# Kernel tuning notes

Measured on AMD Instinct MI355X. Metric: run time of the kernel, lower is better.

## Reference

```python
import jax, jax.numpy as jnp
import numpy as np
import math

B, L, C, H = 8, 1024, 1024, 8
EPS = 1e-5

def setup_inputs() -> dict:
    key = jax.random.key(0)
    ks = jax.random.split(key, 5)
    s = 0.02
    return {
        "x": jax.random.normal(ks[0], (B, L, C), dtype=jnp.float32),
        "ln_g": jnp.ones((C,), dtype=jnp.float32),
        "ln_b": jnp.zeros((C,), dtype=jnp.float32),
        "w_qkv": jax.random.normal(ks[1], (C, 3 * C), dtype=jnp.float32) * s,
        "b_qkv": jax.random.normal(ks[2], (3 * C,), dtype=jnp.float32) * s,
        "w_out": jax.random.normal(ks[3], (C, C), dtype=jnp.float32) * s,
        "b_out": jax.random.normal(ks[4], (C,), dtype=jnp.float32) * s,
    }

def reference(x, ln_g, ln_b, w_qkv, b_qkv, w_out, b_out):
    bs, length, width = x.shape
    ch = width // H
    # LayerNorm over channels
    mu = jnp.mean(x, axis=-1, keepdims=True)
    var = jnp.mean(jnp.square(x - mu), axis=-1, keepdims=True)
    xn = (x - mu) * jax.lax.rsqrt(var + EPS) * ln_g + ln_b
    # fused QKV projection
    qkv = jnp.einsum('blc,cd->bld', xn, w_qkv) + b_qkv  # [B, L, 3C]
    q, k, v = jnp.split(qkv, 3, axis=2)                 # each [B, L, C]
    scale = 1.0 / math.sqrt(math.sqrt(ch))
    # faithful raw row-major reshape as in the torch .view call
    q = (q * scale).reshape(bs * H, length, ch)
    k = (k * scale).reshape(bs * H, length, ch)
    v = v.reshape(bs * H, length, ch)
    w = jnp.einsum('bqc,bkc->bqk', q, k)                # [B*H, L, L] score matrix
    w = jax.nn.softmax(w.astype(jnp.float32), axis=-1).astype(q.dtype)
    attn = jnp.einsum('bqk,bkc->bqc', w, v).reshape(bs, length, -1)
    out = jnp.einsum('blc,cd->bld', attn, w_out) + b_out + xn  # residual uses normalized x
    return out
```

## Files before the change

### kernel.cpp

```cpp
#include <hip/hip_runtime.h>
#include <hip/hip_bf16.h>


typedef __attribute__((ext_vector_type(8))) short short8;
typedef __attribute__((ext_vector_type(4))) float f32x4;

#define QK_SCALE 0.29730177875068026f

__device__ __forceinline__ float bf2f(ushort u) {
    union { float f; unsigned int i; } c; c.i = ((unsigned int)u) << 16; return c.f;
}
__device__ __forceinline__ ushort f2bf(float f) {
    union { float f; unsigned int i; } c; c.f = f;
    unsigned int x = c.i;
    return (ushort)((x + 0x7FFFu + ((x >> 16) & 1u)) >> 16);
}

__device__ __forceinline__ void gload_lds16(const ushort* g, ushort* l) {
    __builtin_amdgcn_global_load_lds(
        (const __attribute__((address_space(1))) unsigned int*)g,
        (__attribute__((address_space(3))) unsigned int*)l, 16, 0, 0);
}

__global__ __launch_bounds__(256) void prep_kernel(
    const float* __restrict__ x, const float* __restrict__ g,
    const float* __restrict__ b, ushort* __restrict__ xn,
    const float* __restrict__ w_qkv, ushort* __restrict__ wqkvT,
    const float* __restrict__ w_out, ushort* __restrict__ woutT) {
    __shared__ ushort t[32][33];
    int bid = blockIdx.x;
    int tid = threadIdx.x;
    if (bid < 2048) {
        int w = tid >> 6, lane = tid & 63;
        int row = bid * 4 + w;
        const float* xr = x + (size_t)row * 1024;
        float v[4][4];
        float s1 = 0.f, s2 = 0.f;
#pragma unroll
        for (int j = 0; j < 4; j++) {
            float4 t4 = *(const float4*)(xr + lane * 4 + j * 256);
            v[j][0] = t4.x; v[j][1] = t4.y; v[j][2] = t4.z; v[j][3] = t4.w;
#pragma unroll
            for (int e = 0; e < 4; e++) { s1 += v[j][e]; s2 += v[j][e] * v[j][e]; }
        }
#pragma unroll
        for (int m = 32; m >= 1; m >>= 1) { s1 += __shfl_xor(s1, m); s2 += __shfl_xor(s2, m); }
        float mu = s1 * (1.0f / 1024.0f);
        float var = s2 * (1.0f / 1024.0f) - mu * mu;
        float rs = rsqrtf(var + 1e-5f);
#pragma unroll
        for (int j = 0; j < 4; j++) {
            int c0 = lane * 4 + j * 256;
            float4 gg = *(const float4*)(g + c0);
            float4 bb = *(const float4*)(b + c0);
            float gA[4] = {gg.x, gg.y, gg.z, gg.w};
            float bA[4] = {bb.x, bb.y, bb.z, bb.w};
            ushort o[4];
#pragma unroll
            for (int e = 0; e < 4; e++) o[e] = f2bf((v[j][e] - mu) * rs * gA[e] + bA[e]);
            uint2 pk;
            pk.x = (uint)o[0] | ((uint)o[1] << 16);
            pk.y = (uint)o[2] | ((uint)o[3] << 16);
            *(uint2*)(xn + (size_t)row * 1024 + c0) = pk;
        }
    } else {
        const float* in; ushort* out; int R, Cc, bx, by;
        if (bid < 5120) {
            int tt = bid - 2048;
            in = w_qkv; out = wqkvT; R = 1024; Cc = 3072;
            bx = (tt % 96) * 32; by = (tt / 96) * 32;
        } else {
            int tt = bid - 5120;
            in = w_out; out = woutT; R = 1024; Cc = 1024;
            bx = (tt % 32) * 32; by = (tt / 32) * 32;
        }
        int tx = tid & 31, ty = tid >> 5;
#pragma unroll
        for (int j = 0; j < 32; j += 8)
            t[ty + j][tx] = f2bf(in[(size_t)(by + ty + j) * Cc + bx + tx]);
        __syncthreads();
#pragma unroll
        for (int j = 0; j < 32; j += 8)
            out[(size_t)(bx + ty + j) * R + by + tx] = t[tx][ty + j];
    }
}

__global__ __launch_bounds__(256) void transpose_head(
    const ushort* __restrict__ in, ushort* __restrict__ out) {
    __shared__ ushort t[32][33];
    int h = blockIdx.z;
    int j0 = blockIdx.y * 32;
    int d0 = blockIdx.x * 32;
    int tx = threadIdx.x & 31, ty = threadIdx.x >> 5;
    const ushort* src = in + (size_t)h * 131072;
    ushort* dst = out + (size_t)h * 131072;
#pragma unroll
    for (int j = 0; j < 32; j += 8)
        t[ty + j][tx] = src[(size_t)(j0 + ty + j) * 128 + d0 + tx];
    __syncthreads();
#pragma unroll
    for (int j = 0; j < 32; j += 8)
        dst[(size_t)(d0 + ty + j) * 1024 + j0 + tx] = t[tx][ty + j];
}

__device__ __forceinline__ void stage8(const ushort* __restrict__ Ab,
                                       const ushort* __restrict__ Bb, int t2,
                                       ushort* AsD, ushort* BsD, int tid) {
    const ushort* As_src = Ab + t2 * 64;
    const ushort* Bs_src = Bb + t2 * 64;
#pragma unroll
    for (int i = 0; i < 4; i++) {
        int lin = i * 256 + tid;
        int r = lin >> 3, p = lin & 7;
        int l = p ^ (r & 7);
        gload_lds16(As_src + (size_t)r * 1024 + l * 8, &AsD[lin * 8]);
    }
#pragma unroll
    for (int i = 0; i < 4; i++) {
        int lin = i * 256 + tid;
        int r = lin >> 3, p = lin & 7;
        int l = p ^ (r & 7);
        gload_lds16(Bs_src + (size_t)r * 1024 + l * 8, &BsD[lin * 8]);
    }
}

__global__ __launch_bounds__(256, 2) void gemm_qkv(
    const ushort* __restrict__ A, const ushort* __restrict__ Bt,
    const float* __restrict__ bias, ushort* __restrict__ out0,
    ushort* __restrict__ out1, ushort* __restrict__ out2) {
    __shared__ __align__(16) ushort As[2][128 * 64];
    __shared__ __align__(16) ushort Bs[2][128 * 64];

    int tid = threadIdx.x;
    int lane = tid & 63, w = tid >> 6;
    int l15 = lane & 15, q4 = lane >> 4;
    int wrM = (w >> 1) * 64;
    int wcN = (w & 1) * 64;

    int bid = blockIdx.x;
    int xcd = bid & 7;
    int i = bid >> 3;
    int by = xcd * 8 + (i & 7);
    int bx = i >> 3;
    int rowBase = by * 128, colBase = bx * 128;

    const ushort* Ab = A + (size_t)rowBase * 1024;
    const ushort* Bb = Bt + (size_t)colBase * 1024;

    f32x4 acc[4][4];
    f32x4 zero = {0.f, 0.f, 0.f, 0.f};
#pragma unroll
    for (int mi = 0; mi < 4; mi++)
#pragma unroll
        for (int ni = 0; ni < 4; ni++) acc[mi][ni] = zero;

    stage8(Ab, Bb, 0, &As[0][0], &Bs[0][0], tid);
    stage8(Ab, Bb, 1, &As[1][0], &Bs[1][0], tid);
    asm volatile("s_waitcnt vmcnt(8)" ::: "memory");
    __builtin_amdgcn_s_barrier();

    for (int t = 0; t < 16; ++t) {
        const int cur = t & 1;
        const ushort* Ac = &As[cur][0];
        const ushort* Bc = &Bs[cur][0];

        short8 aF[4][2], bF[4][2];
#pragma unroll
        for (int kk = 0; kk < 2; kk++) {
#pragma unroll
            for (int mi = 0; mi < 4; mi++) {
                int r = wrM + mi * 16 + l15;
                aF[mi][kk] = *(const short8*)&Ac[r * 64 + ((kk * 4 + q4) ^ (r & 7)) * 8];
            }
#pragma unroll
            for (int ni = 0; ni < 4; ni++) {
                int r = wcN + ni * 16 + l15;
                bF[ni][kk] = *(const short8*)&Bc[r * 64 + ((kk * 4 + q4) ^ (r & 7)) * 8];
            }
        }

        __builtin_amdgcn_s_setprio(1);
#pragma unroll
        for (int mi = 0; mi < 4; mi++)
#pragma unroll
            for (int ni = 0; ni < 4; ni++)
                acc[mi][ni] = __builtin_amdgcn_mfma_f32_16x16x32_bf16(
                    aF[mi][0], bF[ni][0], acc[mi][ni], 0, 0, 0);
        __builtin_amdgcn_s_setprio(0);

        asm volatile("s_waitcnt lgkmcnt(0)" ::: "memory");
        __builtin_amdgcn_s_barrier();
        if (t < 14) stage8(Ab, Bb, t + 2, &As[cur][0], &Bs[cur][0], tid);

        __builtin_amdgcn_s_setprio(1);
#pragma unroll
        for (int mi = 0; mi < 4; mi++)
#pragma unroll
            for (int ni = 0; ni < 4; ni++)
                acc[mi][ni] = __builtin_amdgcn_mfma_f32_16x16x32_bf16(
                    aF[mi][1], bF[ni][1], acc[mi][ni], 0, 0, 0);
        __builtin_amdgcn_s_setprio(0);

        if (t < 15) {
            if (t < 14) asm volatile("s_waitcnt vmcnt(8)" ::: "memory");
            else        asm volatile("s_waitcnt vmcnt(0)" ::: "memory");
            __builtin_amdgcn_s_barrier();
        }
    }

#pragma unroll
    for (int ni = 0; ni < 4; ni++) {
        int col = colBase + wcN + ni * 16 + l15;
        float bv = bias[col];
        float sc = (col < 2048) ? QK_SCALE : 1.0f;
        int bsel = col >> 10, cc = col & 1023;
        ushort* dst = (bsel == 0) ? out0 : ((bsel == 1) ? out1 : out2);
#pragma unroll
        for (int mi = 0; mi < 4; mi++) {
            f32x4 a = acc[mi][ni];
#pragma unroll
            for (int r = 0; r < 4; r++) {
                int row = rowBase + wrM + mi * 16 + q4 * 4 + r;
                dst[(size_t)row * 1024 + cc] = f2bf((a[r] + bv) * sc);
            }
        }
    }
}

__global__ __launch_bounds__(256, 2) void gemm_out(
    const ushort* __restrict__ A, const ushort* __restrict__ Bt,
    const float* __restrict__ bias, const ushort* __restrict__ resid,
    float* __restrict__ outf) {
    __shared__ __align__(16) ushort As[2][128 * 64];
    __shared__ __align__(16) ushort Bs[2][128 * 64];

    int tid = threadIdx.x;
    int lane = tid & 63, w = tid >> 6;
    int l15 = lane & 15, q4 = lane >> 4;
    int wrM = (w >> 1) * 64;
    int wcN = (w & 1) * 64;

    int bid = blockIdx.x;
    int xcd = bid & 7;
    int i = bid >> 3;
    int by = xcd * 8 + (i & 7);
    int bx = i >> 3;
    int rowBase = by * 128, colBase = bx * 128;

    const ushort* Ab = A + (size_t)rowBase * 1024;
    const ushort* Bb = Bt + (size_t)colBase * 1024;

    f32x4 acc[4][4];
    f32x4 zero = {0.f, 0.f, 0.f, 0.f};
#pragma unroll
    for (int mi = 0; mi < 4; mi++)
#pragma unroll
        for (int ni = 0; ni < 4; ni++) acc[mi][ni] = zero;

    stage8(Ab, Bb, 0, &As[0][0], &Bs[0][0], tid);
    stage8(Ab, Bb, 1, &As[1][0], &Bs[1][0], tid);
    asm volatile("s_waitcnt vmcnt(8)" ::: "memory");
    __builtin_amdgcn_s_barrier();

    for (int t = 0; t < 16; ++t) {
        const int cur = t & 1;
        const ushort* Ac = &As[cur][0];
        const ushort* Bc = &Bs[cur][0];

        short8 aF[4][2], bF[4][2];
#pragma unroll
        for (int kk = 0; kk < 2; kk++) {
#pragma unroll
            for (int mi = 0; mi < 4; mi++) {
                int r = wrM + mi * 16 + l15;
                aF[mi][kk] = *(const short8*)&Ac[r * 64 + ((kk * 4 + q4) ^ (r & 7)) * 8];
            }
#pragma unroll
            for (int ni = 0; ni < 4; ni++) {
                int r = wcN + ni * 16 + l15;
                bF[ni][kk] = *(const short8*)&Bc[r * 64 + ((kk * 4 + q4) ^ (r & 7)) * 8];
            }
        }

        __builtin_amdgcn_s_setprio(1);
#pragma unroll
        for (int mi = 0; mi < 4; mi++)
#pragma unroll
            for (int ni = 0; ni < 4; ni++)
                acc[mi][ni] = __builtin_amdgcn_mfma_f32_16x16x32_bf16(
                    aF[mi][0], bF[ni][0], acc[mi][ni], 0, 0, 0);
        __builtin_amdgcn_s_setprio(0);

        asm volatile("s_waitcnt lgkmcnt(0)" ::: "memory");
        __builtin_amdgcn_s_barrier();
        if (t < 14) stage8(Ab, Bb, t + 2, &As[cur][0], &Bs[cur][0], tid);

        __builtin_amdgcn_s_setprio(1);
#pragma unroll
        for (int mi = 0; mi < 4; mi++)
#pragma unroll
            for (int ni = 0; ni < 4; ni++)
                acc[mi][ni] = __builtin_amdgcn_mfma_f32_16x16x32_bf16(
                    aF[mi][1], bF[ni][1], acc[mi][ni], 0, 0, 0);
        __builtin_amdgcn_s_setprio(0);

        if (t < 15) {
            if (t < 14) asm volatile("s_waitcnt vmcnt(8)" ::: "memory");
            else        asm volatile("s_waitcnt vmcnt(0)" ::: "memory");
            __builtin_amdgcn_s_barrier();
        }
    }

#pragma unroll
    for (int ni = 0; ni < 4; ni++) {
        int col = colBase + wcN + ni * 16 + l15;
        float bv = bias[col];
#pragma unroll
        for (int mi = 0; mi < 4; mi++) {
            f32x4 a = acc[mi][ni];
#pragma unroll
            for (int r = 0; r < 4; r++) {
                int row = rowBase + wrM + mi * 16 + q4 * 4 + r;
                outf[(size_t)row * 1024 + col] =
                    a[r] + bv + bf2f(resid[(size_t)row * 1024 + col]);
            }
        }
    }
}

__device__ __forceinline__ void attn_stage(const ushort* __restrict__ Kh,
                                           const ushort* __restrict__ Vh,
                                           int kt, ushort* KsD, ushort* VtD,
                                           int tid) {
#pragma unroll
    for (int i = 0; i < 2; i++) {
        int linear = i * 512 + tid;
        int r = linear >> 4, p = linear & 15;
        int l = p ^ (r & 15);
        gload_lds16(&Kh[(size_t)(kt * 64 + r) * 128 + l * 8], &KsD[linear * 8]);
    }
#pragma unroll
    for (int i = 0; i < 2; i++) {
        int linear = i * 512 + tid;
        int d = linear >> 3, p = linear & 7;
        int c = p ^ (d & 7);
        gload_lds16(&Vh[(size_t)d * 1024 + kt * 64 + c * 8], &VtD[linear * 8]);
    }
}

__global__ __launch_bounds__(512) void attn_kernel(
    const ushort* __restrict__ qb, const ushort* __restrict__ kb,
    const ushort* __restrict__ vt, ushort* __restrict__ ob) {
    int bid = blockIdx.x;
    int xcd = bid & 7, ii = bid >> 3;
    int g = xcd * 8 + (ii >> 3);
    int qblk = ii & 7;
    const ushort* Qh = qb + (size_t)g * 131072;
    const ushort* Kh = kb + (size_t)g * 131072;
    const ushort* Vh = vt + (size_t)g * 131072;

    __shared__ __align__(16) ushort Ks[2][64 * 128];
    __shared__ __align__(16) ushort Vt[2][128 * 64];
    __shared__ __align__(16) ushort Ps[128 * 64];

    int tid = threadIdx.x, lane = tid & 63, w = tid >> 6;
    int l15 = lane & 15, q4 = lane >> 4;
    int q0 = qblk * 128;

    short8 qf[4];
#pragma unroll
    for (int ks = 0; ks < 4; ks++)
        qf[ks] = *(const short8*)&Qh[(size_t)(q0 + w * 16 + l15) * 128 + ks * 32 + q4 * 8];

    f32x4 zero = {0.f, 0.f, 0.f, 0.f};
    f32x4 o[8];
#pragma unroll
    for (int ni = 0; ni < 8; ni++) o[ni] = zero;
    float plsum[4] = {0.f, 0.f, 0.f, 0.f};

    attn_stage(Kh, Vh, 0, &Ks[0][0], &Vt[0][0], tid);
    attn_stage(Kh, Vh, 1, &Ks[1][0], &Vt[1][0], tid);
    asm volatile("s_waitcnt vmcnt(4)" ::: "memory");
    __builtin_amdgcn_s_barrier();

    for (int kt = 0; kt < 16; kt++) {
        const int cur = kt & 1;
        const ushort* Kc = &Ks[cur][0];
        const ushort* Vc = &Vt[cur][0];

        f32x4 sacc[4];
#pragma unroll
        for (int ni = 0; ni < 4; ni++) sacc[ni] = zero;
        __builtin_amdgcn_s_setprio(1);
#pragma unroll
        for (int ks = 0; ks < 4; ks++) {
#pragma unroll
            for (int ni = 0; ni < 4; ni++) {
                int r = ni * 16 + l15;
                int p = (ks * 4 + q4) ^ (r & 15);
                short8 bF = *(const short8*)&Kc[r * 128 + p * 8];
                sacc[ni] = __builtin_amdgcn_mfma_f32_16x16x32_bf16(
                    qf[ks], bF, sacc[ni], 0, 0, 0);
            }
        }
        __builtin_amdgcn_s_setprio(0);

#pragma unroll
        for (int ni = 0; ni < 4; ni++) {
#pragma unroll
            for (int r = 0; r < 4; r++) {
                float pv = __expf(sacc[ni][r]);
                plsum[r] += pv;
                int qloc = w * 16 + q4 * 4 + r;
                int key = ni * 16 + l15;
                int pc = (key >> 3) ^ (qloc & 7);
                Ps[qloc * 64 + pc * 8 + (key & 7)] = f2bf(pv);
            }
        }

        __builtin_amdgcn_s_setprio(1);
#pragma unroll
        for (int ks2 = 0; ks2 < 2; ks2++) {
            int c = ks2 * 4 + q4;
            int row = w * 16 + l15;
            short8 aF = *(const short8*)&Ps[row * 64 + (c ^ (l15 & 7)) * 8];
#pragma unroll
            for (int ni = 0; ni < 8; ni++) {
                int d = ni * 16 + l15;
                short8 bF = *(const short8*)&Vc[d * 64 + (c ^ (d & 7)) * 8];
                o[ni] = __builtin_amdgcn_mfma_f32_16x16x32_bf16(aF, bF, o[ni], 0, 0, 0);
            }
        }
        __builtin_amdgcn_s_setprio(0);

        asm volatile("s_waitcnt lgkmcnt(0)" ::: "memory");
        __builtin_amdgcn_s_barrier();
        if (kt < 14) attn_stage(Kh, Vh, kt + 2, &Ks[cur][0], &Vt[cur][0], tid);
        if (kt < 14)       asm volatile("s_waitcnt vmcnt(4)" ::: "memory");
        else if (kt == 14) asm volatile("s_waitcnt vmcnt(0)" ::: "memory");
        if (kt < 15) __builtin_amdgcn_s_barrier();
    }

#pragma unroll
    for (int r = 0; r < 4; r++) {
#pragma unroll
        for (int m = 1; m < 16; m <<= 1) plsum[r] += __shfl_xor(plsum[r], m, 16);
    }
    float inv[4];
#pragma unroll
    for (int r = 0; r < 4; r++) inv[r] = 1.0f / plsum[r];
#pragma unroll
    for (int ni = 0; ni < 8; ni++)
#pragma unroll
        for (int r = 0; r < 4; r++) {
            int qrow = q0 + w * 16 + q4 * 4 + r;
            ob[(size_t)g * 131072 + (size_t)qrow * 128 + ni * 16 + l15] =
                f2bf(o[ni][r] * inv[r]);
        }
}

extern "C" void kernel_launch(void* const* d_in, const int* in_sizes, int n_in,
                              void* d_out, int out_size, void* d_ws, size_t ws_size,
                              hipStream_t stream) {
    const float* x     = (const float*)d_in[0];
    const float* ln_g  = (const float*)d_in[1];
    const float* ln_b  = (const float*)d_in[2];
    const float* w_qkv = (const float*)d_in[3];
    const float* b_qkv = (const float*)d_in[4];
    const float* w_out = (const float*)d_in[5];
    const float* b_out = (const float*)d_in[6];
    float* out = (float*)d_out;

    const size_t MC = 8192ull * 1024ull;
    ushort* xn    = (ushort*)d_ws;
    ushort* wqkvT = xn + MC;
    ushort* woutT = wqkvT + 3072ull * 1024ull;
    ushort* qbuf  = woutT + 1024ull * 1024ull;
    ushort* kbuf  = qbuf + MC;
    ushort* vtbuf = kbuf + MC;
    ushort* attnb = vtbuf + MC;

    prep_kernel<<<6144, 256, 0, stream>>>(x, ln_g, ln_b, xn, w_qkv, wqkvT, w_out, woutT);
    gemm_qkv<<<1536, 256, 0, stream>>>(xn, wqkvT, b_qkv, qbuf, kbuf, attnb);
    transpose_head<<<dim3(4, 32, 64), 256, 0, stream>>>(attnb, vtbuf);
    attn_kernel<<<512, 512, 0, stream>>>(qbuf, kbuf, vtbuf, attnb);
    gemm_out<<<512, 256, 0, stream>>>(attnb, woutT, b_out, xn, out);
}
```

Before: 239.0 us.

## Fuse V head transpose into attention kernel via register-staged LDS writes

Removes the separate transpose_head kernel and instead loads raw V rows into registers inside the attention kernel, writing them transposed and swizzled into LDS for each key tile. This removes one kernel launch and a full global read/write round trip of the V tensor. In exchange the V path now uses ordinary register loads and scalar 2-byte LDS stores instead of direct global-to-LDS loads, which adds LDS store traffic and register pressure in the attention loop. Output buffers are reassigned so the attention result goes to the former vt buffer.

```diff
diff --git a/kernel.cpp b/kernel.cpp
--- a/kernel.cpp
+++ b/kernel.cpp
@@ -85,24 +85,6 @@
     }
 }
 
-__global__ __launch_bounds__(256) void transpose_head(
-    const ushort* __restrict__ in, ushort* __restrict__ out) {
-    __shared__ ushort t[32][33];
-    int h = blockIdx.z;
-    int j0 = blockIdx.y * 32;
-    int d0 = blockIdx.x * 32;
-    int tx = threadIdx.x & 31, ty = threadIdx.x >> 5;
-    const ushort* src = in + (size_t)h * 131072;
-    ushort* dst = out + (size_t)h * 131072;
-#pragma unroll
-    for (int j = 0; j < 32; j += 8)
-        t[ty + j][tx] = src[(size_t)(j0 + ty + j) * 128 + d0 + tx];
-    __syncthreads();
-#pragma unroll
-    for (int j = 0; j < 32; j += 8)
-        dst[(size_t)(d0 + ty + j) * 1024 + j0 + tx] = t[tx][ty + j];
-}
-
 __device__ __forceinline__ void stage8(const ushort* __restrict__ Ab,
                                        const ushort* __restrict__ Bb, int t2,
                                        ushort* AsD, ushort* BsD, int tid) {
@@ -328,10 +310,8 @@
     }
 }
 
-__device__ __forceinline__ void attn_stage(const ushort* __restrict__ Kh,
-                                           const ushort* __restrict__ Vh,
-                                           int kt, ushort* KsD, ushort* VtD,
-                                           int tid) {
+__device__ __forceinline__ void stageK(const ushort* __restrict__ Kh, int kt,
+                                       ushort* KsD, int tid) {
 #pragma unroll
     for (int i = 0; i < 2; i++) {
         int linear = i * 512 + tid;
@@ -339,25 +319,32 @@
         int l = p ^ (r & 15);
         gload_lds16(&Kh[(size_t)(kt * 64 + r) * 128 + l * 8], &KsD[linear * 8]);
     }
-#pragma unroll
-    for (int i = 0; i < 2; i++) {
-        int linear = i * 512 + tid;
-        int d = linear >> 3, p = linear & 7;
-        int c = p ^ (d & 7);
-        gload_lds16(&Vh[(size_t)d * 1024 + kt * 64 + c * 8], &VtD[linear * 8]);
+}
+
+__device__ __forceinline__ void writeV(ushort* VtD, int vkey, int vd0,
+                                       uint4 lo, uint4 hi) {
+    uint wl[4] = {lo.x, lo.y, lo.z, lo.w};
+    uint wh[4] = {hi.x, hi.y, hi.z, hi.w};
+    int c8 = (vkey >> 3);
+    int k7 = (vkey & 7);
+#pragma unroll
+    for (int j = 0; j < 8; j++) {
+        int d = vd0 + j;
+        int p = (c8 ^ (d & 7)) << 3;
+        VtD[d * 64 + p + k7] = (ushort)(wl[j >> 1] >> ((j & 1) * 16));
+        VtD[(d + 64) * 64 + p + k7] = (ushort)(wh[j >> 1] >> ((j & 1) * 16));
     }
 }
 
 __global__ __launch_bounds__(512) void attn_kernel(
     const ushort* __restrict__ qb, const ushort* __restrict__ kb,
-    const ushort* __restrict__ vt, ushort* __restrict__ ob) {
+    const ushort* __restrict__ vraw, ushort* __restrict__ ob) {
     int bid = blockIdx.x;
     int xcd = bid & 7, ii = bid >> 3;
     int g = xcd * 8 + (ii >> 3);
     int qblk = ii & 7;
     const ushort* Qh = qb + (size_t)g * 131072;
     const ushort* Kh = kb + (size_t)g * 131072;
-    const ushort* Vh = vt + (size_t)g * 131072;
 
     __shared__ __align__(16) ushort Ks[2][64 * 128];
     __shared__ __align__(16) ushort Vt[2][128 * 64];
@@ -367,6 +354,11 @@
     int l15 = lane & 15, q4 = lane >> 4;
     int q0 = qblk * 128;
 
+    int vkey = lane;
+    int vd0 = w * 8;
+    const ushort* vsrc = vraw + (size_t)(128 * g + (vkey >> 3)) * 1024
+                              + (vkey & 7) * 128 + vd0;
+
     short8 qf[4];
 #pragma unroll
     for (int ks = 0; ks < 4; ks++)
@@ -378,9 +370,16 @@
     for (int ni = 0; ni < 8; ni++) o[ni] = zero;
     float plsum[4] = {0.f, 0.f, 0.f, 0.f};
 
-    attn_stage(Kh, Vh, 0, &Ks[0][0], &Vt[0][0], tid);
-    attn_stage(Kh, Vh, 1, &Ks[1][0], &Vt[1][0], tid);
+    uint4 eLo, eHi, oLo, oHi;
+    stageK(Kh, 0, &Ks[0][0], tid);
+    eLo = *(const uint4*)(vsrc);
+    eHi = *(const uint4*)(vsrc + 64);
+    stageK(Kh, 1, &Ks[1][0], tid);
+    oLo = *(const uint4*)(vsrc + 8192);
+    oHi = *(const uint4*)(vsrc + 8192 + 64);
     asm volatile("s_waitcnt vmcnt(4)" ::: "memory");
+    writeV(&Vt[0][0], vkey, vd0, eLo, eHi);
+    asm volatile("s_waitcnt lgkmcnt(0)" ::: "memory");
     __builtin_amdgcn_s_barrier();
 
     for (int kt = 0; kt < 16; kt++) {
@@ -435,10 +434,21 @@
 
         asm volatile("s_waitcnt lgkmcnt(0)" ::: "memory");
         __builtin_amdgcn_s_barrier();
-        if (kt < 14) attn_stage(Kh, Vh, kt + 2, &Ks[cur][0], &Vt[cur][0], tid);
-        if (kt < 14)       asm volatile("s_waitcnt vmcnt(4)" ::: "memory");
-        else if (kt == 14) asm volatile("s_waitcnt vmcnt(0)" ::: "memory");
-        if (kt < 15) __builtin_amdgcn_s_barrier();
+        if (kt < 14) {
+            stageK(Kh, kt + 2, &Ks[cur][0], tid);
+            const ushort* vp = vsrc + (size_t)(kt + 2) * 8192;
+            if (cur == 0) { eLo = *(const uint4*)vp; eHi = *(const uint4*)(vp + 64); }
+            else          { oLo = *(const uint4*)vp; oHi = *(const uint4*)(vp + 64); }
+            asm volatile("s_waitcnt vmcnt(4)" ::: "memory");
+        } else if (kt == 14) {
+            asm volatile("s_waitcnt vmcnt(0)" ::: "memory");
+        }
+        if (kt < 15) {
+            if (cur == 0) writeV(&Vt[1][0], vkey, vd0, oLo, oHi);
+            else          writeV(&Vt[0][0], vkey, vd0, eLo, eHi);
+            asm volatile("s_waitcnt lgkmcnt(0)" ::: "memory");
+            __builtin_amdgcn_s_barrier();
+        }
     }
 
 #pragma unroll
@@ -482,7 +492,6 @@
 
     prep_kernel<<<6144, 256, 0, stream>>>(x, ln_g, ln_b, xn, w_qkv, wqkvT, w_out, woutT);
     gemm_qkv<<<1536, 256, 0, stream>>>(xn, wqkvT, b_qkv, qbuf, kbuf, attnb);
-    transpose_head<<<dim3(4, 32, 64), 256, 0, stream>>>(attnb, vtbuf);
-    attn_kernel<<<512, 512, 0, stream>>>(qbuf, kbuf, vtbuf, attnb);
-    gemm_out<<<512, 256, 0, stream>>>(attnb, woutT, b_out, xn, out);
-}
+    attn_kernel<<<512, 512, 0, stream>>>(qbuf, kbuf, attnb, vtbuf);
+    gemm_out<<<512, 256, 0, stream>>>(vtbuf, woutT, b_out, xn, out);
+}
```

Result: slower. 255.8 us (+7.0%).

## Fuse V transpose into QKV GEMM epilogue and drop transpose kernel

Applied to the files above, without the earlier changes.

The QKV GEMM epilogue now writes V straight into a transposed per-head layout with packed 8-byte stores, so the separate transpose_head kernel launch goes away. The attention kernel's V staging and the P-matrix layout are reindexed so the key ordering matches the permuted V layout. This saves one kernel launch and a full read and write of V. In exchange the GEMM stores become strided column writes, and the P/V index permutation must agree exactly for the result to stay correct.

```diff
diff --git a/kernel.cpp b/kernel.cpp
--- a/kernel.cpp
+++ b/kernel.cpp
@@ -85,24 +85,6 @@
     }
 }
 
-__global__ __launch_bounds__(256) void transpose_head(
-    const ushort* __restrict__ in, ushort* __restrict__ out) {
-    __shared__ ushort t[32][33];
-    int h = blockIdx.z;
-    int j0 = blockIdx.y * 32;
-    int d0 = blockIdx.x * 32;
-    int tx = threadIdx.x & 31, ty = threadIdx.x >> 5;
-    const ushort* src = in + (size_t)h * 131072;
-    ushort* dst = out + (size_t)h * 131072;
-#pragma unroll
-    for (int j = 0; j < 32; j += 8)
-        t[ty + j][tx] = src[(size_t)(j0 + ty + j) * 128 + d0 + tx];
-    __syncthreads();
-#pragma unroll
-    for (int j = 0; j < 32; j += 8)
-        dst[(size_t)(d0 + ty + j) * 1024 + j0 + tx] = t[tx][ty + j];
-}
-
 __device__ __forceinline__ void stage8(const ushort* __restrict__ Ab,
                                        const ushort* __restrict__ Bb, int t2,
                                        ushort* AsD, ushort* BsD, int tid) {
@@ -127,7 +109,7 @@
 __global__ __launch_bounds__(256, 2) void gemm_qkv(
     const ushort* __restrict__ A, const ushort* __restrict__ Bt,
     const float* __restrict__ bias, ushort* __restrict__ out0,
-    ushort* __restrict__ out1, ushort* __restrict__ out2) {
+    ushort* __restrict__ out1, ushort* __restrict__ wv) {
     __shared__ __align__(16) ushort As[2][128 * 64];
     __shared__ __align__(16) ushort Bs[2][128 * 64];
 
@@ -208,20 +190,42 @@
         }
     }
 
-#pragma unroll
-    for (int ni = 0; ni < 4; ni++) {
-        int col = colBase + wcN + ni * 16 + l15;
-        float bv = bias[col];
-        float sc = (col < 2048) ? QK_SCALE : 1.0f;
-        int bsel = col >> 10, cc = col & 1023;
-        ushort* dst = (bsel == 0) ? out0 : ((bsel == 1) ? out1 : out2);
-#pragma unroll
-        for (int mi = 0; mi < 4; mi++) {
-            f32x4 a = acc[mi][ni];
-#pragma unroll
-            for (int r = 0; r < 4; r++) {
-                int row = rowBase + wrM + mi * 16 + q4 * 4 + r;
-                dst[(size_t)row * 1024 + cc] = f2bf((a[r] + bv) * sc);
+    if (colBase < 2048) {
+#pragma unroll
+        for (int ni = 0; ni < 4; ni++) {
+            int col = colBase + wcN + ni * 16 + l15;
+            float bv = bias[col];
+            int cc = col & 1023;
+            ushort* dst = (col < 1024) ? out0 : out1;
+#pragma unroll
+            for (int mi = 0; mi < 4; mi++) {
+                f32x4 a = acc[mi][ni];
+#pragma unroll
+                for (int r = 0; r < 4; r++) {
+                    int row = rowBase + wrM + mi * 16 + q4 * 4 + r;
+                    dst[(size_t)row * 1024 + cc] = f2bf((a[r] + bv) * QK_SCALE);
+                }
+            }
+        }
+    } else {
+        int g = rowBase >> 7;
+        int s7 = (colBase - 2048) >> 7;
+        ushort* Wg = wv + (size_t)g * 131072 + (size_t)s7 * 128;
+#pragma unroll
+        for (int ni = 0; ni < 4; ni++) {
+            int col = colBase + wcN + ni * 16 + l15;
+            float bv = bias[col];
+            int d = wcN + ni * 16 + l15;
+#pragma unroll
+            for (int mi = 0; mi < 4; mi++) {
+                f32x4 a = acc[mi][ni];
+                int off0 = wrM + mi * 16 + q4 * 4;
+                ushort o0 = f2bf(a[0] + bv), o1 = f2bf(a[1] + bv);
+                ushort o2 = f2bf(a[2] + bv), o3 = f2bf(a[3] + bv);
+                uint2 pk;
+                pk.x = (uint)o0 | ((uint)o1 << 16);
+                pk.y = (uint)o2 | ((uint)o3 << 16);
+                *(uint2*)&Wg[(size_t)d * 1024 + off0] = pk;
             }
         }
     }
@@ -329,7 +333,7 @@
 }
 
 __device__ __forceinline__ void attn_stage(const ushort* __restrict__ Kh,
-                                           const ushort* __restrict__ Vh,
+                                           const ushort* __restrict__ Wg,
                                            int kt, ushort* KsD, ushort* VtD,
                                            int tid) {
 #pragma unroll
@@ -344,20 +348,20 @@
         int linear = i * 512 + tid;
         int d = linear >> 3, p = linear & 7;
         int c = p ^ (d & 7);
-        gload_lds16(&Vh[(size_t)d * 1024 + kt * 64 + c * 8], &VtD[linear * 8]);
+        gload_lds16(&Wg[(size_t)d * 1024 + c * 128 + kt * 8], &VtD[linear * 8]);
     }
 }
 
 __global__ __launch_bounds__(512) void attn_kernel(
     const ushort* __restrict__ qb, const ushort* __restrict__ kb,
-    const ushort* __restrict__ vt, ushort* __restrict__ ob) {
+    const ushort* __restrict__ wv, ushort* __restrict__ ob) {
     int bid = blockIdx.x;
     int xcd = bid & 7, ii = bid >> 3;
     int g = xcd * 8 + (ii >> 3);
     int qblk = ii & 7;
     const ushort* Qh = qb + (size_t)g * 131072;
     const ushort* Kh = kb + (size_t)g * 131072;
-    const ushort* Vh = vt + (size_t)g * 131072;
+    const ushort* Wg = wv + (size_t)g * 131072;
 
     __shared__ __align__(16) ushort Ks[2][64 * 128];
     __shared__ __align__(16) ushort Vt[2][128 * 64];
@@ -378,8 +382,8 @@
     for (int ni = 0; ni < 8; ni++) o[ni] = zero;
     float plsum[4] = {0.f, 0.f, 0.f, 0.f};
 
-    attn_stage(Kh, Vh, 0, &Ks[0][0], &Vt[0][0], tid);
-    attn_stage(Kh, Vh, 1, &Ks[1][0], &Vt[1][0], tid);
+    attn_stage(Kh, Wg, 0, &Ks[0][0], &Vt[0][0], tid);
+    attn_stage(Kh, Wg, 1, &Ks[1][0], &Vt[1][0], tid);
     asm volatile("s_waitcnt vmcnt(4)" ::: "memory");
     __builtin_amdgcn_s_barrier();
 
@@ -413,8 +417,8 @@
                 plsum[r] += pv;
                 int qloc = w * 16 + q4 * 4 + r;
                 int key = ni * 16 + l15;
-                int pc = (key >> 3) ^ (qloc & 7);
-                Ps[qloc * 64 + pc * 8 + (key & 7)] = f2bf(pv);
+                int pc = (key & 7) ^ (qloc & 7);
+                Ps[qloc * 64 + pc * 8 + (key >> 3)] = f2bf(pv);
             }
         }
 
@@ -435,7 +439,7 @@
 
         asm volatile("s_waitcnt lgkmcnt(0)" ::: "memory");
         __builtin_amdgcn_s_barrier();
-        if (kt < 14) attn_stage(Kh, Vh, kt + 2, &Ks[cur][0], &Vt[cur][0], tid);
+        if (kt < 14) attn_stage(Kh, Wg, kt + 2, &Ks[cur][0], &Vt[cur][0], tid);
         if (kt < 14)       asm volatile("s_waitcnt vmcnt(4)" ::: "memory");
         else if (kt == 14) asm volatile("s_waitcnt vmcnt(0)" ::: "memory");
         if (kt < 15) __builtin_amdgcn_s_barrier();
@@ -481,8 +485,7 @@
     ushort* attnb = vtbuf + MC;
 
     prep_kernel<<<6144, 256, 0, stream>>>(x, ln_g, ln_b, xn, w_qkv, wqkvT, w_out, woutT);
-    gemm_qkv<<<1536, 256, 0, stream>>>(xn, wqkvT, b_qkv, qbuf, kbuf, attnb);
-    transpose_head<<<dim3(4, 32, 64), 256, 0, stream>>>(attnb, vtbuf);
+    gemm_qkv<<<1536, 256, 0, stream>>>(xn, wqkvT, b_qkv, qbuf, kbuf, vtbuf);
     attn_kernel<<<512, 512, 0, stream>>>(qbuf, kbuf, vtbuf, attnb);
     gemm_out<<<512, 256, 0, stream>>>(attnb, woutT, b_out, xn, out);
 }
```

Measured after the change: 237.1 us. No clear change (-0.8%).
